# Kernel tuning notes

Measured on AMD Instinct MI355X. Metric: run time of the kernel, lower is better.

The kernel has to match this reference:

```python
import jax, jax.numpy as jnp
import numpy as np

LEBESGUE_P = 3          # lebesgue_p from __init__
WEIGHT_RANGE = 0.1      # weight init scale
B, C_IN, H, W = 32, 96, 56, 56
C_OUT, K = 384, 3
STRIDE = (1, 1)
PADDING = ((1, 1), (1, 1))


def setup_inputs() -> dict:
    key = jax.random.key(0)
    kx, kw = jax.random.split(key)
    x = jax.random.normal(kx, (B, C_IN, H, W), dtype=jnp.float32)
    # learned buffer 'weight': [out_channels, in_channels, kH, kW]
    weight = jax.random.normal(kw, (C_OUT, C_IN, K, K), dtype=jnp.float32) * WEIGHT_RANGE
    return {"x": x, "weight": weight}


def reference(x, weight):
    # get_pre_activations: conv with power-transformed weight sign(w)*|w|^(p-1)
    w_eff = jnp.sign(weight) * jnp.abs(weight) ** (LEBESGUE_P - 1)
    pre_x = jax.lax.conv_general_dilated(
        x, w_eff,
        window_strides=STRIDE,
        padding=PADDING,
        dimension_numbers=("NCHW", "OIHW", "NCHW"),
    )  # [B, C_OUT, H, W]

    # get_wta (groups=1): hard winner-take-all over channel dim per (b, h, w).
    # Original transposes/reshapes to [C_OUT, B*H*W], argmax over dim 0, one_hot,
    # then reshapes back; mathematically identical to a channel-axis argmax+one_hot.
    winners = jnp.argmax(pre_x, axis=1)                                   # [B, H, W]
    wta = jax.nn.one_hot(winners, pre_x.shape[1], axis=1, dtype=pre_x.dtype)  # [B, C_OUT, H, W]

    # forward(x, return_x_wta=True) returns (pre_x, wta); stack so output is one array
    return jnp.stack([pre_x, wta], axis=0)  # [2, B, C_OUT, H, W]
```

## Files before the change

### kernel.cpp

```cpp
#include <hip/hip_runtime.h>
#include <math.h>
#include <stdint.h>

#define CIN  96
#define COUT 384
#define HH   56
#define WW   56
#define BB   32

#define MARGIN   2e-3f
#define CAP      32000u
#define WT32_OFF (256 * 1024)
#define WT64_OFF (2 * 1024 * 1024)
#define WT16_OFF (5 * 1024 * 1024)
#define POSB     8

#define HL2      331776
#define XSB      6336

typedef _Float16 half8 __attribute__((ext_vector_type(8)));
typedef float    f32x4 __attribute__((ext_vector_type(4)));

__global__ void prep_wt16(const float* __restrict__ w, _Float16* __restrict__ wt16,
                          uint32_t* __restrict__ cnt) {
    int row = blockIdx.x * blockDim.x + threadIdx.x;
    if (row == 0) *cnt = 0u;
    if (row >= HL2 / 8) return;
    int c16 = row & 15;
    int rem = row >> 4;
    int khw = rem % 9;
    int rem2 = rem / 9;
    int kp  = rem2 % 12;
    int nb  = rem2 / 12;
    int co  = nb * 16 + c16;
    half8 hv, lv;
    #pragma unroll
    for (int j = 0; j < 8; ++j) {
        int ci = kp * 8 + j;
        float wv = w[(size_t)co * (CIN * 9) + ci * 9 + khw];
        double d = (double)wv;
        float ef = (float)(d * fabs(d));
        _Float16 hi = (_Float16)ef;
        hv[j] = hi;
        lv[j] = (_Float16)(ef - (float)hi);
    }
    *(half8*)(wt16 + (size_t)row * 8) = hv;
    *(half8*)(wt16 + HL2 + (size_t)row * 8) = lv;
}

__global__ void prep_wt64(const float* __restrict__ w, double* __restrict__ wt64) {
    int idx = blockIdx.x * blockDim.x + threadIdx.x;
    if (idx >= COUT * CIN * 9) return;
    int r  = idx / COUT;
    int co = idx - r * COUT;
    double d = (double)w[(size_t)co * (CIN * 9) + r];
    wt64[(size_t)r * COUT + co] = d * fabs(d);
}

__global__ void prep_tier2(const float* __restrict__ w, float* __restrict__ wt32,
                           double* __restrict__ wt64, uint32_t* __restrict__ cnt) {
    int idx = blockIdx.x * blockDim.x + threadIdx.x;
    if (idx == 0) *cnt = 0u;
    if (idx >= COUT * CIN * 9) return;
    int r  = idx / COUT;
    int co = idx - r * COUT;
    double d = (double)w[(size_t)co * (CIN * 9) + r];
    double e = d * fabs(d);
    wt64[(size_t)r * COUT + co] = e;
    wt32[(size_t)r * COUT + co] = (float)e;
}

__global__ __launch_bounds__(768, 6)
void conv_mfma(const float* __restrict__ x, const _Float16* __restrict__ wt16,
               float* __restrict__ out, uint32_t* __restrict__ cnt,
               uint32_t* __restrict__ flags) {
    const int h   = blockIdx.x;
    const int b   = blockIdx.y;
    const int tid = threadIdx.x;
    const int l   = tid & 63;
    const int wg  = tid >> 6;
    const int g   = l >> 4;
    const int c   = l & 15;

    __shared__ char lds[37888];
    _Float16* xs  = (_Float16*)lds;
    float4*   red = (float4*)(lds + 25344);
    int*      win = (int*)(lds + 25344 + 12288);

    f32x4 acc[4][2];
    #pragma unroll
    for (int mf = 0; mf < 4; ++mf)
        #pragma unroll
        for (int nf = 0; nf < 2; ++nf)
            #pragma unroll
            for (int q = 0; q < 4; ++q) acc[mf][nf][q] = 0.0f;

    const _Float16* pa0 = xs + (g * 198 + c) * 8;

    auto stage = [&](int chunk) {
        _Float16* xsb = xs + (chunk & 1) * XSB;
        const int ci0 = chunk * 32;
        for (int idx = tid; idx < 4 * 198; idx += 768) {
            int cq  = idx / 198;
            int rem = idx - cq * 198;
            int r   = rem / 66;
            int col = rem - r * 66;
            int gh  = h + r - 1;
            int gw  = col - 1;
            half8 hv = {};
            if ((unsigned)gh < 56u && (unsigned)gw < 56u) {
                const float* px = x + (((size_t)b * CIN + (ci0 + cq * 8)) * HH + gh) * WW + gw;
                #pragma unroll
                for (int i = 0; i < 8; ++i) hv[i] = (_Float16)px[i * 3136];
            }
            *(half8*)(xsb + (size_t)(cq * 198 + rem) * 8) = hv;
        }
    };

    stage(0);
    __syncthreads();

    for (int chunk = 0; chunk < 3; ++chunk) {
        if (chunk < 2) stage(chunk + 1);

        const _Float16* pax = pa0 + (chunk & 1) * XSB;
        const _Float16* pb0 = wt16 + (size_t)(((wg * 2 + 0) * 12 + chunk * 4 + g) * 9) * 128 + c * 8;
        const _Float16* pb1 = wt16 + (size_t)(((wg * 2 + 1) * 12 + chunk * 4 + g) * 9) * 128 + c * 8;

        #pragma unroll
        for (int khw = 0; khw < 9; ++khw) {
            const int kh = khw / 3;
            const int kw = khw - kh * 3;
            half8 B0 = *(const half8*)(pb0 + khw * 128);
            half8 B1 = *(const half8*)(pb1 + khw * 128);
            #pragma unroll
            for (int mf = 0; mf < 4; ++mf) {
                half8 Ah = *(const half8*)(pax + (kh * 66 + mf * 16 + kw) * 8);
                acc[mf][0] = __builtin_amdgcn_mfma_f32_16x16x32_f16(Ah, B0, acc[mf][0], 0, 0, 0);
                acc[mf][1] = __builtin_amdgcn_mfma_f32_16x16x32_f16(Ah, B1, acc[mf][1], 0, 0, 0);
            }
        }
        __syncthreads();
    }

    #pragma unroll
    for (int mf = 0; mf < 4; ++mf) {
        #pragma unroll
        for (int q = 0; q < 4; ++q) {
            float best = acc[mf][0][q];
            int   bco  = wg * 32 + c;
            float sec  = -1e30f;
            {
                float v = acc[mf][1][q];
                if (v > best) { sec = best; best = v; bco = wg * 32 + 16 + c; }
                else sec = v;
            }
            #pragma unroll
            for (int off = 1; off <= 8; off <<= 1) {
                float ov = __shfl_xor(best, off, 64);
                int   oc = __shfl_xor(bco,  off, 64);
                float os = __shfl_xor(sec,  off, 64);
                if (ov > best || (ov == best && oc < bco)) {
                    sec = fmaxf(best, os);
                    best = ov; bco = oc;
                } else {
                    sec = fmaxf(sec, ov);
                }
            }
            if (c == 0) {
                int m = mf * 16 + g * 4 + q;
                red[wg * 64 + m] = make_float4(best, sec, __int_as_float(bco), 0.0f);
            }
        }
    }
    __syncthreads();
    {
        const int m = tid >> 3;
        const int j = tid & 7;
        if (m < 64) {
            float4 a = red[j * 64 + m];
            float best = a.x, sec = a.y;
            int   bco  = __float_as_int(a.z);
            if (j < 4) {
                float4 d = red[(j + 8) * 64 + m];
                if (d.x > best) {
                    sec = fmaxf(best, d.y);
                    best = d.x; bco = __float_as_int(d.z);
                } else {
                    sec = fmaxf(sec, d.x);
                }
            }
            #pragma unroll
            for (int off = 1; off <= 4; off <<= 1) {
                float ov = __shfl_xor(best, off, 64);
                int   oc = __shfl_xor(bco,  off, 64);
                float os = __shfl_xor(sec,  off, 64);
                if (ov > best || (ov == best && oc < bco)) {
                    sec = fmaxf(best, os);
                    best = ov; bco = oc;
                } else {
                    sec = fmaxf(sec, ov);
                }
            }
            if (j == 0 && m < 56) {
                win[m] = bco;
                if ((best - sec) < MARGIN) {
                    uint32_t k = atomicAdd(cnt, 1u);
                    if (k < CAP) flags[k] = (uint32_t)((b * 56 + h) * 56 + m);
                }
            }
        }
    }
    __syncthreads();

    const size_t wta_off = (size_t)BB * COUT * HH * WW;

    if (tid < 56) {
        int co_w = win[tid];
        out[wta_off + ((size_t)(b * COUT + co_w)) * 3136 + (size_t)h * 56 + tid] = 1.0f;
    }

    #pragma unroll
    for (int nf = 0; nf < 2; ++nf) {
        const int co = wg * 32 + nf * 16 + c;
        float* basep = out + ((size_t)(b * COUT + co)) * 3136 + (size_t)h * 56;
        #pragma unroll
        for (int mf = 0; mf < 4; ++mf) {
            const int m0 = mf * 16 + g * 4;
            if (m0 <= 52) {
                f32x4 v;
                #pragma unroll
                for (int q = 0; q < 4; ++q) v[q] = acc[mf][nf][q];
                *(f32x4*)(basep + m0) = v;
            }
        }
    }
}

__global__ __launch_bounds__(512, 2)
void conv_wta_f32(const float* __restrict__ x, const float* __restrict__ wt,
                  float* __restrict__ out, uint32_t* __restrict__ cnt,
                  uint32_t* __restrict__ flags) {
    const int h0  = blockIdx.x * 2;
    const int b   = blockIdx.y;
    const int tid = threadIdx.x;
    const int cg  = tid & 63;
    const int wg  = tid >> 6;
    const int co0 = cg * 6;
    const int ws0 = wg * 7;

    __shared__ float xs[32 * 4 * 58];
    __shared__ int   win[2][56];

    float acc[2][6][7];
    #pragma unroll
    for (int r = 0; r < 2; ++r)
        #pragma unroll
        for (int c = 0; c < 6; ++c)
            #pragma unroll
            for (int i = 0; i < 7; ++i) acc[r][c][i] = 0.0f;

    for (int chunk = 0; chunk < 3; ++chunk) {
        const int ci0 = chunk * 32;
        __syncthreads();
        for (int idx = tid; idx < 32 * 4 * 58; idx += 512) {
            int ci  = idx / 232;
            int rem = idx - ci * 232;
            int r   = rem / 58;
            int c   = rem - r * 58;
            int gh  = h0 + r - 1;
            int gw  = c - 1;
            float v = 0.0f;
            if ((unsigned)gh < 56u && (unsigned)gw < 56u)
                v = x[(((size_t)b * CIN + (ci0 + ci)) * HH + gh) * WW + gw];
            xs[idx] = v;
        }
        __syncthreads();
        for (int ci = 0; ci < 32; ++ci) {
            const int gci = ci0 + ci;
            #pragma unroll
            for (int kh = 0; kh < 3; ++kh) {
                float xa[9], xb[9];
                const float* xr0 = &xs[(ci * 4 + kh) * 58 + ws0];
                const float* xr1 = &xs[(ci * 4 + kh + 1) * 58 + ws0];
                #pragma unroll
                for (int j = 0; j < 9; ++j) { xa[j] = xr0[j]; xb[j] = xr1[j]; }
                #pragma unroll
                for (int kw = 0; kw < 3; ++kw) {
                    const float* p = wt + (size_t)((gci * 3 + kh) * 3 + kw) * COUT + co0;
                    float2 w01 = *(const float2*)(p);
                    float2 w23 = *(const float2*)(p + 2);
                    float2 w45 = *(const float2*)(p + 4);
                    float wd[6] = {w01.x, w01.y, w23.x, w23.y, w45.x, w45.y};
                    #pragma unroll
                    for (int c = 0; c < 6; ++c)
                        #pragma unroll
                        for (int i = 0; i < 7; ++i) {
                            acc[0][c][i] = fmaf(wd[c], xa[i + kw], acc[0][c][i]);
                            acc[1][c][i] = fmaf(wd[c], xb[i + kw], acc[1][c][i]);
                        }
                }
            }
        }
    }

    #pragma unroll
    for (int rr = 0; rr < 2; ++rr) {
        #pragma unroll
        for (int i = 0; i < 7; ++i) {
            float best = acc[rr][0][i];
            int   bco  = co0;
            float sec  = -1e30f;
            #pragma unroll
            for (int c = 1; c < 6; ++c) {
                float v = acc[rr][c][i];
                if (v > best) { sec = best; best = v; bco = co0 + c; }
                else if (v > sec) sec = v;
            }
            #pragma unroll
            for (int off = 32; off > 0; off >>= 1) {
                float ov = __shfl_xor(best, off, 64);
                int   oc = __shfl_xor(bco,  off, 64);
                float os = __shfl_xor(sec,  off, 64);
                if (ov > best || (ov == best && oc < bco)) {
                    sec = fmaxf(best, os);
                    best = ov; bco = oc;
                } else {
                    sec = fmaxf(sec, ov);
                }
            }
            if (cg == 0) {
                win[rr][ws0 + i] = bco;
                if ((best - sec) < MARGIN) {
                    uint32_t k = atomicAdd(cnt, 1u);
                    if (k < CAP) flags[k] = (uint32_t)((b * 56 + (h0 + rr)) * 56 + (ws0 + i));
                }
            }
        }
    }

    const size_t wta_off = (size_t)BB * COUT * HH * WW;
    float* ldsT = xs;
    __syncthreads();
    for (int k = 0; k < 8; ++k) {
        if ((cg >> 3) == k) {
            const int cr = (cg & 7) * 6;
            #pragma unroll
            for (int c = 0; c < 6; ++c)
                #pragma unroll
                for (int rr = 0; rr < 2; ++rr)
                    #pragma unroll
                    for (int i = 0; i < 7; ++i)
                        ldsT[(cr + c) * 113 + rr * 56 + ws0 + i] = acc[rr][c][i];
        }
        __syncthreads();
        for (int l = tid; l < 48 * 112; l += 512) {
            int co_r = l / 112;
            int rem  = l - co_r * 112;
            int rr   = rem / 56;
            int w    = rem - rr * 56;
            int co   = k * 48 + co_r;
            float v  = ldsT[co_r * 113 + rem];
            size_t o = ((size_t)(b * COUT + co)) * 3136 + (size_t)(h0 + rr) * 56 + w;
            out[o] = v;
            out[wta_off + o] = (co == win[rr][w]) ? 1.0f : 0.0f;
        }
        __syncthreads();
    }
}

__global__ __launch_bounds__(384)
void fixup_f64(const float* __restrict__ x, const double* __restrict__ wt64,
               float* __restrict__ out, const uint32_t* __restrict__ cnt,
               const uint32_t* __restrict__ flags) {
    __shared__ float  xp[POSB][CIN * 9];
    __shared__ double sv[POSB][COUT];
    __shared__ int winners[POSB];

    uint32_t n = *cnt;
    if (n > CAP) n = CAP;
    const int tid = threadIdx.x;
    const int wg  = tid >> 6;
    const int lane = tid & 63;
    const size_t wta_off = (size_t)BB * COUT * HH * WW;

    for (uint32_t base = blockIdx.x * POSB; base < n; base += gridDim.x * POSB) {
        int np = (int)(n - base) < POSB ? (int)(n - base) : POSB;
        __syncthreads();
        for (int idx = tid; idx < np * CIN * 9; idx += 384) {
            int p  = idx / (CIN * 9);
            int r  = idx - p * (CIN * 9);
            int ci = r / 9;
            int k  = r - ci * 9;
            int kh = k / 3, kw = k - kh * 3;
            uint32_t pos = flags[base + p];
            int w_ = pos % 56;
            int h_ = (pos / 56) % 56;
            int b_ = pos / 3136;
            int gh = h_ + kh - 1, gw = w_ + kw - 1;
            float v = 0.0f;
            if ((unsigned)gh < 56u && (unsigned)gw < 56u)
                v = x[(((size_t)b_ * CIN + ci) * HH + gh) * WW + gw];
            xp[p][r] = v;
        }
        __syncthreads();
        {
            const int co = tid;
            double a[POSB];
            #pragma unroll
            for (int p = 0; p < POSB; ++p) a[p] = 0.0;
            #pragma unroll 4
            for (int r = 0; r < CIN * 9; ++r) {
                double wd = wt64[(size_t)r * COUT + co];
                #pragma unroll
                for (int p = 0; p < POSB; ++p)
                    a[p] = fma(wd, (double)xp[p][r], a[p]);
            }
            #pragma unroll
            for (int p = 0; p < POSB; ++p) sv[p][co] = a[p];
        }
        __syncthreads();
        for (int p = wg; p < np; p += 6) {
            double best = sv[p][lane * 6];
            int bco = lane * 6;
            #pragma unroll
            for (int c = 1; c < 6; ++c) {
                double v2 = sv[p][lane * 6 + c];
                if (v2 > best) { best = v2; bco = lane * 6 + c; }
            }
            #pragma unroll
            for (int off = 32; off > 0; off >>= 1) {
                double ov = __shfl_xor(best, off, 64);
                int    oc = __shfl_xor(bco,  off, 64);
                if (ov > best || (ov == best && oc < bco)) { best = ov; bco = oc; }
            }
            if (lane == 0) winners[p] = bco;
        }
        __syncthreads();
        for (int idx = tid; idx < np * COUT; idx += 384) {
            int p  = idx / COUT;
            int co = idx - p * COUT;
            uint32_t pos = flags[base + p];
            int w_ = pos % 56;
            int h_ = (pos / 56) % 56;
            int b_ = pos / 3136;
            size_t o = (((size_t)b_ * COUT + co) * HH + h_) * WW + w_;
            out[o] = (float)sv[p][co];
            out[wta_off + o] = (co == winners[p]) ? 1.0f : 0.0f;
        }
        __syncthreads();
    }
}

__global__ __launch_bounds__(256, 2)
void conv_wta_f64(const float* __restrict__ x, const float* __restrict__ wraw,
                  float* __restrict__ out) {
    const int whalf = blockIdx.x;
    const int h     = blockIdx.y;
    const int b     = blockIdx.z;
    const int tid   = threadIdx.x;
    const int cg    = tid & 63;
    const int wg    = tid >> 6;
    const int co0   = cg * 6;
    const int wbase = whalf * 28 + wg * 7;

    __shared__ float xs[32 * 3 * 30];
    double acc[6][7];
    #pragma unroll
    for (int c = 0; c < 6; ++c)
        #pragma unroll
        for (int i = 0; i < 7; ++i) acc[c][i] = 0.0;

    for (int chunk = 0; chunk < 3; ++chunk) {
        const int ci0 = chunk * 32;
        __syncthreads();
        for (int idx = tid; idx < 32 * 3 * 30; idx += 256) {
            int ci = idx / 90, rem = idx - ci * 90;
            int r = rem / 30, c = rem - r * 30;
            int gh = h + r - 1, gw = whalf * 28 - 1 + c;
            float v = 0.0f;
            if ((unsigned)gh < 56u && (unsigned)gw < 56u)
                v = x[(((size_t)b * CIN + (ci0 + ci)) * HH + gh) * WW + gw];
            xs[idx] = v;
        }
        __syncthreads();
        for (int ci = 0; ci < 32; ++ci) {
            const int gci = ci0 + ci;
            #pragma unroll
            for (int kh = 0; kh < 3; ++kh) {
                double xd[9];
                #pragma unroll
                for (int j = 0; j < 9; ++j)
                    xd[j] = (double)xs[(ci * 3 + kh) * 30 + wg * 7 + j];
                #pragma unroll
                for (int kw = 0; kw < 3; ++kw) {
                    #pragma unroll
                    for (int c = 0; c < 6; ++c) {
                        double d = (double)wraw[(size_t)(co0 + c) * (CIN * 9) + gci * 9 + kh * 3 + kw];
                        double wd = d * fabs(d);
                        #pragma unroll
                        for (int i = 0; i < 7; ++i)
                            acc[c][i] = fma(wd, xd[i + kw], acc[c][i]);
                    }
                }
            }
        }
    }
    const size_t wta_off = (size_t)BB * COUT * HH * WW;
    #pragma unroll
    for (int i = 0; i < 7; ++i) {
        double best = acc[0][i];
        int bco = co0;
        #pragma unroll
        for (int c = 1; c < 6; ++c)
            if (acc[c][i] > best) { best = acc[c][i]; bco = co0 + c; }
        #pragma unroll
        for (int off = 32; off > 0; off >>= 1) {
            double ov = __shfl_xor(best, off, 64);
            int    oc = __shfl_xor(bco,  off, 64);
            if (ov > best || (ov == best && oc < bco)) { best = ov; bco = oc; }
        }
        const int w = wbase + i;
        #pragma unroll
        for (int c = 0; c < 6; ++c) {
            size_t o = (((size_t)b * COUT + (co0 + c)) * HH + h) * WW + w;
            out[o] = (float)acc[c][i];
            out[wta_off + o] = (co0 + c == bco) ? 1.0f : 0.0f;
        }
    }
}

extern "C" void kernel_launch(void* const* d_in, const int* in_sizes, int n_in,
                              void* d_out, int out_size, void* d_ws, size_t ws_size,
                              hipStream_t stream) {
    (void)in_sizes; (void)n_in; (void)out_size;
    const float* x = (const float*)d_in[0];
    const float* w = (const float*)d_in[1];
    float* out = (float*)d_out;

    const size_t need16 = (size_t)WT16_OFF + (size_t)2 * HL2 * sizeof(_Float16);
    const size_t need64 = (size_t)WT64_OFF + (size_t)COUT * CIN * 9 * sizeof(double);
    const size_t plane  = (size_t)BB * COUT * HH * WW;

    uint32_t* cnt   = (uint32_t*)d_ws;
    uint32_t* flags = (uint32_t*)((char*)d_ws + 256);
    float*    wt32  = (float*)((char*)d_ws + WT32_OFF);
    double*   wt64  = (double*)((char*)d_ws + WT64_OFF);
    _Float16* wt16  = (_Float16*)((char*)d_ws + WT16_OFF);

    if (ws_size >= need16) {
        hipMemsetAsync(out + plane, 0, plane * sizeof(float), stream);
        prep_wt16<<<(HL2 / 8 + 255) / 256, 256, 0, stream>>>(w, wt16, cnt);
        prep_wt64<<<(COUT * CIN * 9 + 255) / 256, 256, 0, stream>>>(w, wt64);
        conv_mfma<<<dim3(56, 32), 768, 0, stream>>>(x, wt16, out, cnt, flags);
        fixup_f64<<<256, 384, 0, stream>>>(x, wt64, out, cnt, flags);
    } else if (ws_size >= need64) {
        prep_tier2<<<(COUT * CIN * 9 + 255) / 256, 256, 0, stream>>>(w, wt32, wt64, cnt);
        conv_wta_f32<<<dim3(28, 32), 512, 0, stream>>>(x, wt32, out, cnt, flags);
        fixup_f64<<<256, 384, 0, stream>>>(x, wt64, out, cnt, flags);
    } else {
        conv_wta_f64<<<dim3(2, 56, 32), 256, 0, stream>>>(x, w, out);
    }
}
```

Before: 295.7 us.

## Fuse one-hot plane zeroing into conv kernel and merge weight prep kernels

New measurement: 327.9 us. 1.11x slower.

```diff
diff --git a/kernel.cpp b/kernel.cpp
--- a/kernel.cpp
+++ b/kernel.cpp
@@ -21,53 +21,39 @@
 typedef _Float16 half8 __attribute__((ext_vector_type(8)));
 typedef float    f32x4 __attribute__((ext_vector_type(4)));
 
-__global__ void prep_wt16(const float* __restrict__ w, _Float16* __restrict__ wt16,
-                          uint32_t* __restrict__ cnt) {
-    int row = blockIdx.x * blockDim.x + threadIdx.x;
-    if (row == 0) *cnt = 0u;
-    if (row >= HL2 / 8) return;
-    int c16 = row & 15;
-    int rem = row >> 4;
-    int khw = rem % 9;
-    int rem2 = rem / 9;
-    int kp  = rem2 % 12;
-    int nb  = rem2 / 12;
-    int co  = nb * 16 + c16;
-    half8 hv, lv;
-    #pragma unroll
-    for (int j = 0; j < 8; ++j) {
-        int ci = kp * 8 + j;
-        float wv = w[(size_t)co * (CIN * 9) + ci * 9 + khw];
-        double d = (double)wv;
-        float ef = (float)(d * fabs(d));
-        _Float16 hi = (_Float16)ef;
-        hv[j] = hi;
-        lv[j] = (_Float16)(ef - (float)hi);
-    }
-    *(half8*)(wt16 + (size_t)row * 8) = hv;
-    *(half8*)(wt16 + HL2 + (size_t)row * 8) = lv;
-}
-
-__global__ void prep_wt64(const float* __restrict__ w, double* __restrict__ wt64) {
-    int idx = blockIdx.x * blockDim.x + threadIdx.x;
-    if (idx >= COUT * CIN * 9) return;
-    int r  = idx / COUT;
-    int co = idx - r * COUT;
-    double d = (double)w[(size_t)co * (CIN * 9) + r];
-    wt64[(size_t)r * COUT + co] = d * fabs(d);
-}
-
-__global__ void prep_tier2(const float* __restrict__ w, float* __restrict__ wt32,
-                           double* __restrict__ wt64, uint32_t* __restrict__ cnt) {
+__global__ void prep_all(const float* __restrict__ w, _Float16* __restrict__ wt16,
+                         double* __restrict__ wt64, uint32_t* __restrict__ cnt) {
     int idx = blockIdx.x * blockDim.x + threadIdx.x;
     if (idx == 0) *cnt = 0u;
-    if (idx >= COUT * CIN * 9) return;
-    int r  = idx / COUT;
-    int co = idx - r * COUT;
-    double d = (double)w[(size_t)co * (CIN * 9) + r];
-    double e = d * fabs(d);
-    wt64[(size_t)r * COUT + co] = e;
-    wt32[(size_t)r * COUT + co] = (float)e;
+    if (idx < COUT * CIN * 9) {
+        int r  = idx / COUT;
+        int co = idx - r * COUT;
+        double d = (double)w[(size_t)co * (CIN * 9) + r];
+        wt64[(size_t)r * COUT + co] = d * fabs(d);
+    }
+    if (idx < HL2 / 8) {
+        int row = idx;
+        int c16 = row & 15;
+        int rem = row >> 4;
+        int khw = rem % 9;
+        int rem2 = rem / 9;
+        int kp  = rem2 % 12;
+        int nb  = rem2 / 12;
+        int co  = nb * 16 + c16;
+        half8 hv, lv;
+        #pragma unroll
+        for (int j = 0; j < 8; ++j) {
+            int ci = kp * 8 + j;
+            float wv = w[(size_t)co * (CIN * 9) + ci * 9 + khw];
+            double d = (double)wv;
+            float ef = (float)(d * fabs(d));
+            _Float16 hi = (_Float16)ef;
+            hv[j] = hi;
+            lv[j] = (_Float16)(ef - (float)hi);
+        }
+        *(half8*)(wt16 + (size_t)row * 8) = hv;
+        *(half8*)(wt16 + HL2 + (size_t)row * 8) = lv;
+    }
 }
 
 __global__ __launch_bounds__(768, 6)
@@ -86,6 +72,20 @@
     _Float16* xs  = (_Float16*)lds;
     float4*   red = (float4*)(lds + 25344);
     int*      win = (int*)(lds + 25344 + 12288);
+
+    const size_t wta_off = (size_t)BB * COUT * HH * WW;
+
+    {
+        float4* wbase = (float4*)(out + wta_off + (size_t)b * COUT * 3136 + (size_t)h * 56);
+        f32x4 z = {0.f, 0.f, 0.f, 0.f};
+        #pragma unroll
+        for (int k = 0; k < 7; ++k) {
+            int id = tid + k * 768;
+            int co = id / 14;
+            int j  = id - co * 14;
+            *(f32x4*)((float*)wbase + (size_t)co * 3136 + j * 4) = z;
+        }
+    }
 
     f32x4 acc[4][2];
     #pragma unroll
@@ -213,8 +213,6 @@
     }
     __syncthreads();
 
-    const size_t wta_off = (size_t)BB * COUT * HH * WW;
-
     if (tid < 56) {
         int co_w = win[tid];
         out[wta_off + ((size_t)(b * COUT + co_w)) * 3136 + (size_t)h * 56 + tid] = 1.0f;
@@ -235,6 +233,19 @@
             }
         }
     }
+}
+
+__global__ void prep_tier2(const float* __restrict__ w, float* __restrict__ wt32,
+                           double* __restrict__ wt64, uint32_t* __restrict__ cnt) {
+    int idx = blockIdx.x * blockDim.x + threadIdx.x;
+    if (idx == 0) *cnt = 0u;
+    if (idx >= COUT * CIN * 9) return;
+    int r  = idx / COUT;
+    int co = idx - r * COUT;
+    double d = (double)w[(size_t)co * (CIN * 9) + r];
+    double e = d * fabs(d);
+    wt64[(size_t)r * COUT + co] = e;
+    wt32[(size_t)r * COUT + co] = (float)e;
 }
 
 __global__ __launch_bounds__(512, 2)
@@ -540,7 +551,6 @@
 
     const size_t need16 = (size_t)WT16_OFF + (size_t)2 * HL2 * sizeof(_Float16);
     const size_t need64 = (size_t)WT64_OFF + (size_t)COUT * CIN * 9 * sizeof(double);
-    const size_t plane  = (size_t)BB * COUT * HH * WW;
 
     uint32_t* cnt   = (uint32_t*)d_ws;
     uint32_t* flags = (uint32_t*)((char*)d_ws + 256);
@@ -549,9 +559,7 @@
     _Float16* wt16  = (_Float16*)((char*)d_ws + WT16_OFF);
 
     if (ws_size >= need16) {
-        hipMemsetAsync(out + plane, 0, plane * sizeof(float), stream);
-        prep_wt16<<<(HL2 / 8 + 255) / 256, 256, 0, stream>>>(w, wt16, cnt);
-        prep_wt64<<<(COUT * CIN * 9 + 255) / 256, 256, 0, stream>>>(w, wt64);
+        prep_all<<<(COUT * CIN * 9 + 255) / 256, 256, 0, stream>>>(w, wt16, wt64, cnt);
         conv_mfma<<<dim3(56, 32), 768, 0, stream>>>(x, wt16, out, cnt, flags);
         fixup_f64<<<256, 384, 0, stream>>>(x, wt64, out, cnt, flags);
     } else if (ws_size >= need64) {
```
